# Kernel optimization log

Measured on AMD Instinct MI355X. Metric: run time of the kernel, lower is better.

The kernel has to match this reference:

```python
import jax, jax.numpy as jnp
import numpy as np

N_RAYS = 4096
WORLD_LEN = 160
K0_DIM = 12
WIDTH = 128
VIEWPE = 4
BG_LEN = 0.2
XYZ_MIN = -1.0 - BG_LEN
XYZ_MAX = 1.0 + BG_LEN
ALPHA_INIT = 1e-4
ACT_SHIFT = float(np.log(1.0 / (1.0 - ALPHA_INIT) - 1.0))  # density bias shift
BG = 1.0  # background color (render_kwargs['bg'])
DIM0 = 3 + 3 * VIEWPE * 2 + K0_DIM  # 39


def grid_interp(grid, pts):
    """Trilinear interpolation (align_corners=True). grid: [C,R,R,R], pts: [M,3] world coords -> [M,C]."""
    R = grid.shape[1]
    g = (pts - XYZ_MIN) / (XYZ_MAX - XYZ_MIN) * (R - 1)
    g = jnp.clip(g, 0.0, R - 1)
    g0 = jnp.clip(jnp.floor(g).astype(jnp.int32), 0, R - 2)
    f = g - g0
    x0, y0, z0 = g0[:, 0], g0[:, 1], g0[:, 2]
    fx, fy, fz = f[:, 0], f[:, 1], f[:, 2]

    def gat(i, j, k):
        return grid[:, i, j, k]  # [C, M]

    c00 = gat(x0, y0, z0) * (1 - fz) + gat(x0, y0, z0 + 1) * fz
    c01 = gat(x0, y0 + 1, z0) * (1 - fz) + gat(x0, y0 + 1, z0 + 1) * fz
    c10 = gat(x0 + 1, y0, z0) * (1 - fz) + gat(x0 + 1, y0, z0 + 1) * fz
    c11 = gat(x0 + 1, y0 + 1, z0) * (1 - fz) + gat(x0 + 1, y0 + 1, z0 + 1) * fz
    c0 = c00 * (1 - fy) + c01 * fy
    c1 = c10 * (1 - fy) + c11 * fy
    return (c0 * (1 - fx) + c1 * fx).T  # [M, C]


def setup_inputs() -> dict:
    key = jax.random.key(0)
    ks = jax.random.split(key, 11)
    return {
        "rays_o": jax.random.normal(ks[0], (N_RAYS, 3), jnp.float32) * 0.3,
        "rays_d": jax.random.normal(ks[1], (N_RAYS, 3), jnp.float32),
        "viewdirs": jax.random.normal(ks[2], (N_RAYS, 3), jnp.float32),
        "density_grid": jax.random.normal(ks[3], (1, WORLD_LEN, WORLD_LEN, WORLD_LEN), jnp.float32),
        "k0_grid": jax.random.normal(ks[4], (K0_DIM, WORLD_LEN, WORLD_LEN, WORLD_LEN), jnp.float32),
        "w0": jax.random.normal(ks[5], (DIM0, WIDTH), jnp.float32) * 0.05,
        "b0": jnp.zeros((WIDTH,), jnp.float32),
        "w1": jax.random.normal(ks[6], (WIDTH, WIDTH), jnp.float32) * 0.05,
        "b1": jnp.zeros((WIDTH,), jnp.float32),
        "w2": jax.random.normal(ks[7], (WIDTH, 3), jnp.float32) * 0.05,
        "b2": jnp.zeros((3,), jnp.float32),
        "stepsize": 1,
    }


def reference(rays_o, rays_d, viewdirs, density_grid, k0_grid, w0, b0, w1, b1, w2, b2, stepsize):
    sqrt3 = float(np.sqrt(3.0))
    # --- sample_ray: sample points along rays in the contracted domain ---
    N_inner = int(2.0 / (2.0 + 2.0 * BG_LEN) * sqrt3 * WORLD_LEN / stepsize) + 1
    N_outer = int(N_inner * max(0.01, BG_LEN / 2.0))
    b_inner = jnp.linspace(0.0, 2.0 * sqrt3, N_inner + 1)
    b_outer = 2.0 * sqrt3 / jnp.linspace(1.0, 0.001, N_outer + 1)
    t = jnp.concatenate([(b_inner[1:] + b_inner[:-1]) * 0.5,
                         (b_outer[1:] + b_outer[:-1]) * 0.5])  # [P]
    # scene_center = 0, scene_radius = 1 for xyz_min=-1, xyz_max=1
    rd = rays_d / jnp.linalg.norm(rays_d, axis=-1, keepdims=True)
    pts = rays_o[:, None, :] + rd[:, None, :] * t[None, :, None]  # [N,P,3]
    norm = jnp.max(jnp.abs(pts), axis=-1, keepdims=True)
    safe = jnp.maximum(norm, 1e-9)
    pts = jnp.where(norm <= 1.0, pts, pts / safe * (1.0 + BG_LEN - BG_LEN / safe))
    N, P = pts.shape[0], pts.shape[1]
    flat = pts.reshape(-1, 3)  # [M,3]

    # --- density -> alpha (Raw2Alpha); mask_cache is all-True, fast_color_thres=0 ---
    interval = float(stepsize) * 1.0  # voxel_size_ratio == 1
    dens = grid_interp(density_grid, flat)[:, 0].reshape(N, P)
    alpha = 1.0 - jnp.power(1.0 + jnp.exp(dens + ACT_SHIFT), -interval)

    # --- Alphas2Weights: per-ray alpha compositing ---
    T = jnp.cumprod(1.0 - alpha, axis=1)
    T_excl = jnp.concatenate([jnp.ones((N, 1), T.dtype), T[:, :-1]], axis=1)
    weights = alpha * T_excl  # [N,P]
    alphainv_last = T[:, -1]  # [N]

    # --- k0 features + view-dependent MLP ---
    k0 = grid_interp(k0_grid, flat).reshape(N, P, K0_DIM)
    vf = (2.0 ** jnp.arange(VIEWPE)).astype(rays_o.dtype)
    ve = (viewdirs[..., None] * vf).reshape(N, -1)
    vemb = jnp.concatenate([viewdirs, jnp.sin(ve), jnp.cos(ve)], axis=-1)  # [N, 3+24]
    feat = jnp.concatenate(
        [k0, jnp.broadcast_to(vemb[:, None, :], (N, P, vemb.shape[-1]))], axis=-1)  # [N,P,39]
    h = jax.nn.relu(feat @ w0 + b0)
    h = jax.nn.relu(h @ w1 + b1)
    rgb = jax.nn.sigmoid(h @ w2 + b2)  # [N,P,3]

    # --- volume rendering ---
    rgb_marched = jnp.sum(weights[..., None] * rgb, axis=1) + alphainv_last[:, None] * BG
    return rgb_marched  # [N,3]
```

## Files before the change

kernel.cpp:

```cpp
#include <hip/hip_runtime.h>

#define NRAYS 4096
#define PSAMP 254
#define NIN   231
#define GR    160
#define GR2   25600
#define GR3   4096000
#define SROW  136

typedef __attribute__((ext_vector_type(8))) short bf16x8;
typedef __attribute__((ext_vector_type(8))) _Float16 f16x8;
typedef __attribute__((ext_vector_type(2))) _Float16 h2;
typedef __attribute__((ext_vector_type(4))) float f32x4;

__device__ __forceinline__ unsigned short f2bf(float x) {
    union { float f; unsigned u; } v; v.f = x;
    return (unsigned short)((v.u + 0x7fffu + ((v.u >> 16) & 1u)) >> 16);
}
__device__ __forceinline__ float sigmoidf_(float x) { return 1.0f / (1.0f + __expf(-x)); }

__device__ __forceinline__ unsigned packh2(float a, float b) {
    union { _Float16 h; unsigned short u; } ua, ub;
    ua.h = (_Float16)a; ub.h = (_Float16)b;
    return (unsigned)ua.u | ((unsigned)ub.u << 16);
}
__device__ __forceinline__ float h2f(unsigned u16) {
    union { unsigned short u; _Float16 h; } v; v.u = (unsigned short)u16;
    return (float)v.h;
}
__device__ __forceinline__ unsigned pkrtz(float a, float b) {
    unsigned r;
    asm("v_cvt_pkrtz_f16_f32 %0, %1, %2" : "=v"(r) : "v"(a), "v"(b));
    return r;
}
__device__ __forceinline__ h2 u2h(unsigned u) {
    union { unsigned u; h2 h; } v; v.u = u; return v.h;
}

__global__ void prepack(const float* __restrict__ w, unsigned short* __restrict__ out,
                        int K, int N, int ldw, int NT, int KS, int f16mode) {
    const int idx = blockIdx.x * 256 + threadIdx.x;
    if (idx >= NT * KS * 64) return;
    const int l  = idx & 63, f = idx >> 6;
    const int ks = f % KS,  nt = f / KS;
    const int n  = nt * 16 + (l & 15);
    const int k0 = ks * 32 + (l >> 4) * 8;
    unsigned p[4];
    #pragma unroll
    for (int q = 0; q < 4; q++) {
        const int ka = k0 + 2 * q, kb = ka + 1;
        const float va = (ka < K && n < N) ? w[ka * ldw + n] : 0.0f;
        const float vb = (kb < K && n < N) ? w[kb * ldw + n] : 0.0f;
        p[q] = f16mode ? packh2(va, vb)
                       : ((unsigned)f2bf(va) | ((unsigned)f2bf(vb) << 16));
    }
    uint4 v; v.x = p[0]; v.y = p[1]; v.z = p[2]; v.w = p[3];
    ((uint4*)out)[idx] = v;
}

__global__ __launch_bounds__(256) void repack_grid(
    const float* __restrict__ dg, const float* __restrict__ k0g,
    unsigned short* __restrict__ pg)
{
    const int i2 = blockIdx.x * 256 + threadIdx.x;
    if (i2 >= GR3 / 2) return;
    unsigned ow[16];
    #pragma unroll
    for (int c = 0; c < 12; c += 2) {
        const float2 va = ((const float2*)(k0g + (size_t)c       * GR3))[i2];
        const float2 vb = ((const float2*)(k0g + (size_t)(c + 1) * GR3))[i2];
        ow[(c >> 1)]     = packh2(va.x, vb.x);
        ow[8 + (c >> 1)] = packh2(va.y, vb.y);
    }
    const float2 dv = ((const float2*)dg)[i2];
    ow[6]  = packh2(dv.x, 0.0f);
    ow[14] = packh2(dv.y, 0.0f);
    ow[7] = 0u; ow[15] = 0u;
    uint4* dst = (uint4*)(pg + (size_t)i2 * 32);
    dst[0] = make_uint4(ow[0],  ow[1],  ow[2],  ow[3]);
    dst[1] = make_uint4(ow[4],  ow[5],  ow[6],  ow[7]);
    dst[2] = make_uint4(ow[8],  ow[9],  ow[10], ow[11]);
    dst[3] = make_uint4(ow[12], ow[13], ow[14], ow[15]);
}

__global__ __launch_bounds__(256, 2) void voxgo_mfma_pk(
    const float* __restrict__ rays_o, const float* __restrict__ rays_d,
    const float* __restrict__ viewdirs,
    const unsigned short* __restrict__ pg,
    const float* __restrict__ b0, const float* __restrict__ b1,
    const float* __restrict__ b2,
    const unsigned short* __restrict__ pw0, const unsigned short* __restrict__ pw1,
    const unsigned short* __restrict__ pw2,
    float* __restrict__ out)
{
    const int r    = blockIdx.x;
    const int tid  = threadIdx.x;
    const int wv   = tid >> 6, lane = tid & 63, quad = lane >> 4, l16 = lane & 15;

    __shared__ unsigned short hbuf[4][64 * 128];
    __shared__ float wgt[256];
    __shared__ float redbuf[4 * 16 * 3];
    __shared__ float wtot[4];

    const float ox = rays_o[3*r+0], oy = rays_o[3*r+1], oz = rays_o[3*r+2];
    float dxv = rays_d[3*r+0], dyv = rays_d[3*r+1], dzv = rays_d[3*r+2];
    const float vdx = viewdirs[3*r+0], vdy = viewdirs[3*r+1], vdz = viewdirs[3*r+2];
    const float rinv = rsqrtf(dxv*dxv + dyv*dyv + dzv*dzv);
    dxv *= rinv; dyv *= rinv; dzv *= rinv;

    float t;
    if (tid < NIN) {
        t = ((float)tid + 0.5f) * (2.0f * 1.7320508075688772f / 231.0f);
    } else {
        const float lstep = 0.999f / 23.0f;
        const int j = tid - NIN;
        const float L0 = 1.0f - (float)j * lstep;
        const float L1 = 1.0f - (float)(j+1) * lstep;
        t = 1.7320508075688772f * (1.0f/L0 + 1.0f/L1);
    }

    float px = fmaf(dxv, t, ox), py = fmaf(dyv, t, oy), pz = fmaf(dzv, t, oz);
    const float nrm = fmaxf(fabsf(px), fmaxf(fabsf(py), fabsf(pz)));
    if (nrm > 1.0f) {
        const float s = (1.2f - 0.2f / nrm) / nrm;
        px *= s; py *= s; pz *= s;
    }

    const float gsc = 159.0f / 2.4f;
    const float gx = fminf(fmaxf((px + 1.2f) * gsc, 0.0f), 159.0f);
    const float gy = fminf(fmaxf((py + 1.2f) * gsc, 0.0f), 159.0f);
    const float gz = fminf(fmaxf((pz + 1.2f) * gsc, 0.0f), 159.0f);
    const int x0 = min((int)gx, GR-2), y0 = min((int)gy, GR-2), z0 = min((int)gz, GR-2);
    const float fx = gx - (float)x0, fy = gy - (float)y0, fz = gz - (float)z0;
    const int base = x0*GR2 + y0*GR + z0;

    const unsigned short* cp = pg + (size_t)base * 16;
    uint4 hi[8], lo[8];
    #pragma unroll
    for (int j = 0; j < 8; j++) {
        const int off = ((j >> 2) * GR2 + ((j >> 1) & 1) * GR + (j & 1)) * 16;
        hi[j] = *((const uint4*)(cp + off) + 1);
    }
    #pragma unroll
    for (int j = 0; j < 8; j++) {
        const int off = ((j >> 2) * GR2 + ((j >> 1) & 1) * GR + (j & 1)) * 16;
        lo[j] = *((const uint4*)(cp + off));
    }

    float vv[28];
    vv[0] = vdx; vv[1] = vdy; vv[2] = vdz;
    #pragma unroll
    for (int p = 0; p < 4; p++) {
        const float f = (float)(1 << p);
        vv[3+p]  = __sinf(vdx*f);  vv[7+p]  = __sinf(vdy*f);  vv[11+p] = __sinf(vdz*f);
        vv[15+p] = __cosf(vdx*f);  vv[19+p] = __cosf(vdy*f);  vv[23+p] = __cosf(vdz*f);
    }
    vv[27] = 0.0f;

    float dcr[8];
    #pragma unroll
    for (int j = 0; j < 8; j++) dcr[j] = h2f(hi[j].z & 0xffffu);
    const float c00 = dcr[0]*(1.0f-fz) + dcr[1]*fz;
    const float c01 = dcr[2]*(1.0f-fz) + dcr[3]*fz;
    const float c10 = dcr[4]*(1.0f-fz) + dcr[5]*fz;
    const float c11 = dcr[6]*(1.0f-fz) + dcr[7]*fz;
    const float dens = (c00*(1.0f-fy) + c01*fy)*(1.0f-fx) + (c10*(1.0f-fy) + c11*fy)*fx;

    const float ACT_SHIFT = -9.21024036697535f;
    const float alpha = (tid < PSAMP) ? sigmoidf_(dens + ACT_SHIFT) : 0.0f;

    float vscan = 1.0f - alpha;
    #pragma unroll
    for (int off = 1; off < 64; off <<= 1) {
        const float u = __shfl_up(vscan, off);
        if (lane >= off) vscan *= u;
    }
    if (lane == 63) wtot[wv] = vscan;
    __syncthreads();
    float pre = 1.0f;
    #pragma unroll
    for (int w = 0; w < 3; w++) if (w < wv) pre *= wtot[w];
    const float eprev = __shfl_up(vscan, 1);
    const float T_excl = (lane == 0) ? pre : pre * eprev;
    wgt[tid] = alpha * T_excl;

    const float wx0 = 1.0f-fx, wy0 = 1.0f-fy, wz0 = 1.0f-fz;
    h2 wpk[8];
    #pragma unroll
    for (int j = 0; j < 8; j++) {
        const float wj = ((j & 4) ? fx : wx0) * ((j & 2) ? fy : wy0) * ((j & 1) ? fz : wz0);
        const _Float16 wh = (_Float16)wj;
        h2 w2v; w2v[0] = wh; w2v[1] = wh; wpk[j] = w2v;
    }
    h2 ap[6];
    #pragma unroll
    for (int p = 0; p < 6; p++) { h2 z; z[0] = (_Float16)0.0f; z[1] = (_Float16)0.0f; ap[p] = z; }
    #pragma unroll
    for (int j = 0; j < 8; j++) {
        ap[0] += wpk[j] * u2h(lo[j].x);
        ap[1] += wpk[j] * u2h(lo[j].y);
        ap[2] += wpk[j] * u2h(lo[j].z);
        ap[3] += wpk[j] * u2h(lo[j].w);
        ap[4] += wpk[j] * u2h(hi[j].x);
        ap[5] += wpk[j] * u2h(hi[j].y);
    }

    unsigned fw[32];
    #pragma unroll
    for (int p = 0; p < 6; p++) { union { h2 h; unsigned u; } v; v.h = ap[p]; fw[p] = v.u; }
    #pragma unroll
    for (int i = 0; i < 14; i++) fw[6+i] = pkrtz(vv[2*i], vv[2*i+1]);
    #pragma unroll
    for (int i = 20; i < 32; i++) fw[i] = 0u;

    unsigned short* hb = &hbuf[wv][0];
    const unsigned swr = (unsigned)((l16 & 7) << 4);
    {
        const int row = tid & 63;
        const unsigned sw = (unsigned)((row & 7) << 4);
        #pragma unroll
        for (int i = 0; i < 8; i++) {
            uint4 v; v.x = fw[4*i]; v.y = fw[4*i+1]; v.z = fw[4*i+2]; v.w = fw[4*i+3];
            *(uint4*)((char*)hb + row*256 + ((unsigned)(i*16) ^ sw)) = v;
        }
    }

    f32x4 acc1[8][4];
    #pragma unroll
    for (int ft = 0; ft < 8; ft++) {
        const f32x4 bv = *(const f32x4*)(b0 + ft*16 + quad*4);
        #pragma unroll
        for (int st = 0; st < 4; st++) acc1[ft][st] = bv;
    }
    #pragma unroll
    for (int ks = 0; ks < 2; ks++) {
        f16x8 bfr[4];
        #pragma unroll
        for (int st = 0; st < 4; st++)
            bfr[st] = *(const f16x8*)((char*)hb + (st*16 + l16)*256
                                      + ((unsigned)(ks*64 + quad*16) ^ swr));
        #pragma unroll
        for (int ft = 0; ft < 8; ft++) {
            const f16x8 afr = *(const f16x8*)(pw0 + ((ft*2 + ks)*64 + lane)*8);
            #pragma unroll
            for (int st = 0; st < 4; st++)
                acc1[ft][st] = __builtin_amdgcn_mfma_f32_16x16x32_f16(afr, bfr[st], acc1[ft][st], 0,0,0);
        }
    }
    #pragma unroll
    for (int ft = 0; ft < 8; ft++)
        #pragma unroll
        for (int st = 0; st < 4; st++) {
            const f32x4 a = acc1[ft][st];
            uint2 v;
            v.x = pkrtz(fmaxf(a[0], 0.0f), fmaxf(a[1], 0.0f));
            v.y = pkrtz(fmaxf(a[2], 0.0f), fmaxf(a[3], 0.0f));
            *(uint2*)((char*)hb + (st*16 + l16)*256 + ((unsigned)(ft*32 + quad*8) ^ swr)) = v;
        }

    f32x4 acc2[8][4];
    #pragma unroll
    for (int ft = 0; ft < 8; ft++) {
        const f32x4 bv = *(const f32x4*)(b1 + ft*16 + quad*4);
        #pragma unroll
        for (int st = 0; st < 4; st++) acc2[ft][st] = bv;
    }
    #pragma unroll
    for (int ks = 0; ks < 4; ks++) {
        f16x8 bfr[4];
        #pragma unroll
        for (int st = 0; st < 4; st++)
            bfr[st] = *(const f16x8*)((char*)hb + (st*16 + l16)*256
                                      + ((unsigned)(ks*64 + quad*16) ^ swr));
        #pragma unroll
        for (int ft = 0; ft < 8; ft++) {
            const f16x8 afr = *(const f16x8*)(pw1 + ((ft*4 + ks)*64 + lane)*8);
            #pragma unroll
            for (int st = 0; st < 4; st++)
                acc2[ft][st] = __builtin_amdgcn_mfma_f32_16x16x32_f16(afr, bfr[st], acc2[ft][st], 0,0,0);
        }
    }
    #pragma unroll
    for (int ft = 0; ft < 8; ft++)
        #pragma unroll
        for (int st = 0; st < 4; st++) {
            const f32x4 a = acc2[ft][st];
            uint2 v;
            v.x = pkrtz(fmaxf(a[0], 0.0f), fmaxf(a[1], 0.0f));
            v.y = pkrtz(fmaxf(a[2], 0.0f), fmaxf(a[3], 0.0f));
            *(uint2*)((char*)hb + (st*16 + l16)*256 + ((unsigned)(ft*32 + quad*8) ^ swr)) = v;
        }

    f32x4 acc3[4];
    {
        f32x4 bz3; bz3[0] = b2[0]; bz3[1] = b2[1]; bz3[2] = b2[2]; bz3[3] = 0.0f;
        #pragma unroll
        for (int st = 0; st < 4; st++) acc3[st] = bz3;
    }
    #pragma unroll
    for (int ks = 0; ks < 4; ks++) {
        const f16x8 afr = *(const f16x8*)(pw2 + (ks*64 + lane)*8);
        #pragma unroll
        for (int st = 0; st < 4; st++) {
            const f16x8 bfr = *(const f16x8*)((char*)hb + (st*16 + l16)*256
                                              + ((unsigned)(ks*64 + quad*16) ^ swr));
            acc3[st] = __builtin_amdgcn_mfma_f32_16x16x32_f16(afr, bfr, acc3[st], 0,0,0);
        }
    }

    if (quad == 0) {
        float c0 = 0.0f, c1 = 0.0f, c2 = 0.0f;
        #pragma unroll
        for (int st = 0; st < 4; st++) {
            const float w = wgt[wv*64 + st*16 + l16];
            c0 += w * sigmoidf_(acc3[st][0]);
            c1 += w * sigmoidf_(acc3[st][1]);
            c2 += w * sigmoidf_(acc3[st][2]);
        }
        float* rb = &redbuf[(wv*16 + l16)*3];
        rb[0] = c0; rb[1] = c1; rb[2] = c2;
    }
    __syncthreads();
    if (tid < 3) {
        float acc_o = wtot[0]*wtot[1]*wtot[2]*wtot[3];
        #pragma unroll 4
        for (int i = 0; i < 64; i++) acc_o += redbuf[i*3 + tid];
        out[3*r + tid] = acc_o;
    }
}

__global__ __launch_bounds__(256, 2) void voxgo_mfma_f32(
    const float* __restrict__ rays_o, const float* __restrict__ rays_d,
    const float* __restrict__ viewdirs, const float* __restrict__ dg,
    const float* __restrict__ k0g,
    const float* __restrict__ b0, const float* __restrict__ b1,
    const float* __restrict__ b2,
    const unsigned short* __restrict__ pw0, const unsigned short* __restrict__ pw1,
    const unsigned short* __restrict__ pw2,
    float* __restrict__ out)
{
    const int r    = blockIdx.x;
    const int tid  = threadIdx.x;
    const int wv   = tid >> 6, lane = tid & 63, quad = lane >> 4, l16 = lane & 15;

    __shared__ unsigned short hbuf[4][64 * SROW];
    __shared__ float sc[256];
    __shared__ float wgt[256];
    __shared__ float redbuf[256];

    const float ox = rays_o[3*r+0], oy = rays_o[3*r+1], oz = rays_o[3*r+2];
    float dxv = rays_d[3*r+0], dyv = rays_d[3*r+1], dzv = rays_d[3*r+2];
    const float vdx = viewdirs[3*r+0], vdy = viewdirs[3*r+1], vdz = viewdirs[3*r+2];
    const float rinv = rsqrtf(dxv*dxv + dyv*dyv + dzv*dzv);
    dxv *= rinv; dyv *= rinv; dzv *= rinv;

    float t;
    if (tid < NIN) {
        t = ((float)tid + 0.5f) * (2.0f * 1.7320508075688772f / 231.0f);
    } else {
        const float lstep = 0.999f / 23.0f;
        const int j = tid - NIN;
        const float L0 = 1.0f - (float)j * lstep;
        const float L1 = 1.0f - (float)(j+1) * lstep;
        t = 1.7320508075688772f * (1.0f/L0 + 1.0f/L1);
    }

    float px = fmaf(dxv, t, ox), py = fmaf(dyv, t, oy), pz = fmaf(dzv, t, oz);
    const float nrm = fmaxf(fabsf(px), fmaxf(fabsf(py), fabsf(pz)));
    if (nrm > 1.0f) {
        const float s = (1.2f - 0.2f / nrm) / nrm;
        px *= s; py *= s; pz *= s;
    }

    const float gsc = 159.0f / 2.4f;
    const float gx = fminf(fmaxf((px + 1.2f) * gsc, 0.0f), 159.0f);
    const float gy = fminf(fmaxf((py + 1.2f) * gsc, 0.0f), 159.0f);
    const float gz = fminf(fmaxf((pz + 1.2f) * gsc, 0.0f), 159.0f);
    const int x0 = min((int)gx, GR-2), y0 = min((int)gy, GR-2), z0 = min((int)gz, GR-2);
    const float fx = gx - (float)x0, fy = gy - (float)y0, fz = gz - (float)z0;
    const int base = x0*GR2 + y0*GR + z0;

    const float d000 = dg[base],        d001 = dg[base+1];
    const float d010 = dg[base+GR],     d011 = dg[base+GR+1];
    const float d100 = dg[base+GR2],    d101 = dg[base+GR2+1];
    const float d110 = dg[base+GR2+GR], d111 = dg[base+GR2+GR+1];
    const float c00 = d000*(1.0f-fz) + d001*fz;
    const float c01 = d010*(1.0f-fz) + d011*fz;
    const float c10 = d100*(1.0f-fz) + d101*fz;
    const float c11 = d110*(1.0f-fz) + d111*fz;
    const float dens = (c00*(1.0f-fy) + c01*fy)*(1.0f-fx) + (c10*(1.0f-fy) + c11*fy)*fx;

    const float ACT_SHIFT = -9.21024036697535f;
    const float alpha = (tid < PSAMP) ? sigmoidf_(dens + ACT_SHIFT) : 0.0f;

    sc[tid] = 1.0f - alpha;
    __syncthreads();
    #pragma unroll
    for (int off = 1; off < 256; off <<= 1) {
        const float v = (tid >= off) ? sc[tid - off] : 1.0f;
        __syncthreads();
        sc[tid] *= v;
        __syncthreads();
    }
    const float T_excl = (tid == 0) ? 1.0f : sc[tid-1];
    wgt[tid] = alpha * T_excl;

    const float wx0 = 1.0f-fx, wy0 = 1.0f-fy, wz0 = 1.0f-fz;
    const float w000 = wx0*wy0*wz0, w001 = wx0*wy0*fz, w010 = wx0*fy*wz0, w011 = wx0*fy*fz;
    const float w100 = fx*wy0*wz0,  w101 = fx*wy0*fz,  w110 = fx*fy*wz0,  w111 = fx*fy*fz;

    float fv[40];
    #pragma unroll
    for (int c = 0; c < 12; c++) {
        const float* g = k0g + c*GR3 + base;
        fv[c] = w000*g[0]      + w001*g[1]
              + w010*g[GR]     + w011*g[GR+1]
              + w100*g[GR2]    + w101*g[GR2+1]
              + w110*g[GR2+GR] + w111*g[GR2+GR+1];
    }
    fv[12] = vdx; fv[13] = vdy; fv[14] = vdz;
    #pragma unroll
    for (int p = 0; p < 4; p++) {
        const float f = (float)(1 << p);
        fv[15+p] = __sinf(vdx*f);  fv[19+p] = __sinf(vdy*f);  fv[23+p] = __sinf(vdz*f);
        fv[27+p] = __cosf(vdx*f);  fv[31+p] = __cosf(vdy*f);  fv[35+p] = __cosf(vdz*f);
    }
    fv[39] = 0.0f;

    unsigned short* hb = &hbuf[wv][0];
    {
        const int row = tid & 63;
        uint4* dst = (uint4*)(hb + row * SROW);
        #pragma unroll
        for (int i = 0; i < 8; i++) {
            unsigned p[4];
            #pragma unroll
            for (int q = 0; q < 4; q++) {
                const int e0 = i*8 + 2*q, e1 = e0 + 1;
                const unsigned lov = (e0 < 39) ? f2bf(fv[e0]) : 0u;
                const unsigned hiv = (e1 < 39) ? f2bf(fv[e1]) : 0u;
                p[q] = lov | (hiv << 16);
            }
            uint4 v; v.x = p[0]; v.y = p[1]; v.z = p[2]; v.w = p[3];
            dst[i] = v;
        }
    }
    __syncthreads();

    f32x4 acc1[4][8];
    #pragma unroll
    for (int nt = 0; nt < 8; nt++) {
        const float bz = b0[nt*16 + l16];
        #pragma unroll
        for (int mt = 0; mt < 4; mt++) { f32x4 z = {bz,bz,bz,bz}; acc1[mt][nt] = z; }
    }
    #pragma unroll
    for (int ks = 0; ks < 2; ks++) {
        bf16x8 a[4];
        #pragma unroll
        for (int mt = 0; mt < 4; mt++)
            a[mt] = *(const bf16x8*)(hb + (mt*16 + l16)*SROW + ks*32 + quad*8);
        #pragma unroll
        for (int nt = 0; nt < 8; nt++) {
            const bf16x8 b = *(const bf16x8*)(pw0 + ((nt*2 + ks)*64 + lane)*8);
            #pragma unroll
            for (int mt = 0; mt < 4; mt++)
                acc1[mt][nt] = __builtin_amdgcn_mfma_f32_16x16x32_bf16(a[mt], b, acc1[mt][nt], 0,0,0);
        }
    }
    #pragma unroll
    for (int mt = 0; mt < 4; mt++)
        #pragma unroll
        for (int nt = 0; nt < 8; nt++)
            #pragma unroll
            for (int e = 0; e < 4; e++)
                hb[(mt*16 + quad*4 + e)*SROW + nt*16 + l16] = f2bf(fmaxf(acc1[mt][nt][e], 0.0f));
    __syncthreads();

    f32x4 acc2[4][8];
    #pragma unroll
    for (int nt = 0; nt < 8; nt++) {
        const float bz = b1[nt*16 + l16];
        #pragma unroll
        for (int mt = 0; mt < 4; mt++) { f32x4 z = {bz,bz,bz,bz}; acc2[mt][nt] = z; }
    }
    #pragma unroll
    for (int ks = 0; ks < 4; ks++) {
        bf16x8 a[4];
        #pragma unroll
        for (int mt = 0; mt < 4; mt++)
            a[mt] = *(const bf16x8*)(hb + (mt*16 + l16)*SROW + ks*32 + quad*8);
        #pragma unroll
        for (int nt = 0; nt < 8; nt++) {
            const bf16x8 b = *(const bf16x8*)(pw1 + ((nt*4 + ks)*64 + lane)*8);
            #pragma unroll
            for (int mt = 0; mt < 4; mt++)
                acc2[mt][nt] = __builtin_amdgcn_mfma_f32_16x16x32_bf16(a[mt], b, acc2[mt][nt], 0,0,0);
        }
    }
    #pragma unroll
    for (int mt = 0; mt < 4; mt++)
        #pragma unroll
        for (int nt = 0; nt < 8; nt++)
            #pragma unroll
            for (int e = 0; e < 4; e++)
                hb[(mt*16 + quad*4 + e)*SROW + nt*16 + l16] = f2bf(fmaxf(acc2[mt][nt][e], 0.0f));
    __syncthreads();

    f32x4 acc3[4];
    {
        const float bz = (l16 < 3) ? b2[l16] : 0.0f;
        #pragma unroll
        for (int mt = 0; mt < 4; mt++) { f32x4 z = {bz,bz,bz,bz}; acc3[mt] = z; }
    }
    #pragma unroll
    for (int ks = 0; ks < 4; ks++) {
        const bf16x8 b = *(const bf16x8*)(pw2 + (ks*64 + lane)*8);
        #pragma unroll
        for (int mt = 0; mt < 4; mt++) {
            const bf16x8 a = *(const bf16x8*)(hb + (mt*16 + l16)*SROW + ks*32 + quad*8);
            acc3[mt] = __builtin_amdgcn_mfma_f32_16x16x32_bf16(a, b, acc3[mt], 0,0,0);
        }
    }

    float contrib = 0.0f;
    #pragma unroll
    for (int mt = 0; mt < 4; mt++)
        #pragma unroll
        for (int e = 0; e < 4; e++) {
            const float s = sigmoidf_(acc3[mt][e]);
            contrib += wgt[wv*64 + mt*16 + quad*4 + e] * s;
        }
    redbuf[tid] = contrib;
    __syncthreads();
    if (tid < 3) {
        float acc_o = sc[PSAMP-1];
        #pragma unroll
        for (int w = 0; w < 4; w++)
            #pragma unroll
            for (int q = 0; q < 4; q++)
                acc_o += redbuf[w*64 + q*16 + tid];
        out[3*r + tid] = acc_o;
    }
}

extern "C" void kernel_launch(void* const* d_in, const int* in_sizes, int n_in,
                              void* d_out, int out_size, void* d_ws, size_t ws_size,
                              hipStream_t stream) {
    (void)in_sizes; (void)n_in; (void)out_size;
    const size_t PG_BYTES = (size_t)GR3 * 32;
    const size_t PW_BYTES = (size_t)(16 + 32 + 4) * 64 * 8 * 2;

    if (ws_size >= PG_BYTES + PW_BYTES) {
        unsigned short* pg  = (unsigned short*)d_ws;
        unsigned short* pw0 = (unsigned short*)((char*)d_ws + PG_BYTES);
        unsigned short* pw1 = pw0 + 16*64*8;
        unsigned short* pw2 = pw1 + 32*64*8;

        repack_grid<<<GR3/512, 256, 0, stream>>>(
            (const float*)d_in[3], (const float*)d_in[4], pg);
        prepack<<<4, 256, 0, stream>>>((const float*)d_in[5], pw0,  39, 128, 128, 8, 2, 1);
        prepack<<<8, 256, 0, stream>>>((const float*)d_in[7], pw1, 128, 128, 128, 8, 4, 1);
        prepack<<<1, 256, 0, stream>>>((const float*)d_in[9], pw2, 128,   3,   3, 1, 4, 1);

        voxgo_mfma_pk<<<NRAYS, 256, 0, stream>>>(
            (const float*)d_in[0], (const float*)d_in[1], (const float*)d_in[2],
            pg,
            (const float*)d_in[6], (const float*)d_in[8], (const float*)d_in[10],
            pw0, pw1, pw2,
            (float*)d_out);
    } else {
        unsigned short* pw0 = (unsigned short*)d_ws;
        unsigned short* pw1 = pw0 + 16*64*8;
        unsigned short* pw2 = pw1 + 32*64*8;

        prepack<<<4, 256, 0, stream>>>((const float*)d_in[5], pw0,  39, 128, 128, 8, 2, 0);
        prepack<<<8, 256, 0, stream>>>((const float*)d_in[7], pw1, 128, 128, 128, 8, 4, 0);
        prepack<<<1, 256, 0, stream>>>((const float*)d_in[9], pw2, 128,   3,   3, 1, 4, 0);

        voxgo_mfma_f32<<<NRAYS, 256, 0, stream>>>(
            (const float*)d_in[0], (const float*)d_in[1], (const float*)d_in[2],
            (const float*)d_in[3], (const float*)d_in[4],
            (const float*)d_in[6], (const float*)d_in[8], (const float*)d_in[10],
            pw0, pw1, pw2,
            (float*)d_out);
    }
}
```

Measured before the change: 440.7 us.

## Process MLP in two 32-sample halves per wave to halve LDS and registers

Each wave now runs the three-layer MFMA MLP in two passes over 32 samples instead of one pass over 64. This halves the per-wave LDS activation buffer and the accumulator register arrays, and launch bounds are raised from 2 to 4 blocks per CU to use the freed resources for higher occupancy. The cost is twice as many loads of the weight fragments from global memory, less MFMA work per weight load, and some lanes idling while each half writes its inputs.

```diff
diff --git a/kernel.cpp b/kernel.cpp
--- a/kernel.cpp
+++ b/kernel.cpp
@@ -83,7 +83,7 @@
     dst[3] = make_uint4(ow[12], ow[13], ow[14], ow[15]);
 }
 
-__global__ __launch_bounds__(256, 2) void voxgo_mfma_pk(
+__global__ __launch_bounds__(256, 4) void voxgo_mfma_pk(
     const float* __restrict__ rays_o, const float* __restrict__ rays_d,
     const float* __restrict__ viewdirs,
     const unsigned short* __restrict__ pg,
@@ -97,7 +97,7 @@
     const int tid  = threadIdx.x;
     const int wv   = tid >> 6, lane = tid & 63, quad = lane >> 4, l16 = lane & 15;
 
-    __shared__ unsigned short hbuf[4][64 * 128];
+    __shared__ unsigned short hbuf[4][32 * 128];
     __shared__ float wgt[256];
     __shared__ float redbuf[4 * 16 * 3];
     __shared__ float wtot[4];
@@ -205,120 +205,127 @@
         ap[5] += wpk[j] * u2h(hi[j].y);
     }
 
-    unsigned fw[32];
+    unsigned fw[20];
     #pragma unroll
     for (int p = 0; p < 6; p++) { union { h2 h; unsigned u; } v; v.h = ap[p]; fw[p] = v.u; }
     #pragma unroll
     for (int i = 0; i < 14; i++) fw[6+i] = pkrtz(vv[2*i], vv[2*i+1]);
-    #pragma unroll
-    for (int i = 20; i < 32; i++) fw[i] = 0u;
 
     unsigned short* hb = &hbuf[wv][0];
     const unsigned swr = (unsigned)((l16 & 7) << 4);
-    {
-        const int row = tid & 63;
-        const unsigned sw = (unsigned)((row & 7) << 4);
-        #pragma unroll
-        for (int i = 0; i < 8; i++) {
-            uint4 v; v.x = fw[4*i]; v.y = fw[4*i+1]; v.z = fw[4*i+2]; v.w = fw[4*i+3];
-            *(uint4*)((char*)hb + row*256 + ((unsigned)(i*16) ^ sw)) = v;
-        }
-    }
-
-    f32x4 acc1[8][4];
-    #pragma unroll
-    for (int ft = 0; ft < 8; ft++) {
-        const f32x4 bv = *(const f32x4*)(b0 + ft*16 + quad*4);
-        #pragma unroll
-        for (int st = 0; st < 4; st++) acc1[ft][st] = bv;
-    }
-    #pragma unroll
-    for (int ks = 0; ks < 2; ks++) {
-        f16x8 bfr[4];
-        #pragma unroll
-        for (int st = 0; st < 4; st++)
-            bfr[st] = *(const f16x8*)((char*)hb + (st*16 + l16)*256
-                                      + ((unsigned)(ks*64 + quad*16) ^ swr));
+    float cr0 = 0.0f, cr1 = 0.0f, cr2 = 0.0f;
+
+    #pragma unroll
+    for (int p = 0; p < 2; p++) {
+        if ((lane >> 5) == p) {
+            const int row = lane & 31;
+            const unsigned sw = (unsigned)((row & 7) << 4);
+            char* db = (char*)hb + row * 256;
+            #pragma unroll
+            for (int i = 0; i < 5; i++) {
+                uint4 v; v.x = fw[4*i]; v.y = fw[4*i+1]; v.z = fw[4*i+2]; v.w = fw[4*i+3];
+                *(uint4*)(db + ((unsigned)(i*16) ^ sw)) = v;
+            }
+            const uint4 z = make_uint4(0u, 0u, 0u, 0u);
+            #pragma unroll
+            for (int i = 5; i < 8; i++)
+                *(uint4*)(db + ((unsigned)(i*16) ^ sw)) = z;
+        }
+
+        f32x4 acc1[8][2];
         #pragma unroll
         for (int ft = 0; ft < 8; ft++) {
-            const f16x8 afr = *(const f16x8*)(pw0 + ((ft*2 + ks)*64 + lane)*8);
-            #pragma unroll
-            for (int st = 0; st < 4; st++)
-                acc1[ft][st] = __builtin_amdgcn_mfma_f32_16x16x32_f16(afr, bfr[st], acc1[ft][st], 0,0,0);
-        }
-    }
-    #pragma unroll
-    for (int ft = 0; ft < 8; ft++)
-        #pragma unroll
-        for (int st = 0; st < 4; st++) {
-            const f32x4 a = acc1[ft][st];
-            uint2 v;
-            v.x = pkrtz(fmaxf(a[0], 0.0f), fmaxf(a[1], 0.0f));
-            v.y = pkrtz(fmaxf(a[2], 0.0f), fmaxf(a[3], 0.0f));
-            *(uint2*)((char*)hb + (st*16 + l16)*256 + ((unsigned)(ft*32 + quad*8) ^ swr)) = v;
-        }
-
-    f32x4 acc2[8][4];
-    #pragma unroll
-    for (int ft = 0; ft < 8; ft++) {
-        const f32x4 bv = *(const f32x4*)(b1 + ft*16 + quad*4);
-        #pragma unroll
-        for (int st = 0; st < 4; st++) acc2[ft][st] = bv;
-    }
-    #pragma unroll
-    for (int ks = 0; ks < 4; ks++) {
-        f16x8 bfr[4];
-        #pragma unroll
-        for (int st = 0; st < 4; st++)
-            bfr[st] = *(const f16x8*)((char*)hb + (st*16 + l16)*256
-                                      + ((unsigned)(ks*64 + quad*16) ^ swr));
+            const f32x4 bv = *(const f32x4*)(b0 + ft*16 + quad*4);
+            acc1[ft][0] = bv; acc1[ft][1] = bv;
+        }
+        #pragma unroll
+        for (int ks = 0; ks < 2; ks++) {
+            f16x8 bfr[2];
+            #pragma unroll
+            for (int st = 0; st < 2; st++)
+                bfr[st] = *(const f16x8*)((char*)hb + (st*16 + l16)*256
+                                          + ((unsigned)(ks*64 + quad*16) ^ swr));
+            #pragma unroll
+            for (int ft = 0; ft < 8; ft++) {
+                const f16x8 afr = *(const f16x8*)(pw0 + ((ft*2 + ks)*64 + lane)*8);
+                #pragma unroll
+                for (int st = 0; st < 2; st++)
+                    acc1[ft][st] = __builtin_amdgcn_mfma_f32_16x16x32_f16(afr, bfr[st], acc1[ft][st], 0,0,0);
+            }
+        }
+        #pragma unroll
+        for (int ft = 0; ft < 8; ft++)
+            #pragma unroll
+            for (int st = 0; st < 2; st++) {
+                const f32x4 a = acc1[ft][st];
+                uint2 v;
+                v.x = pkrtz(fmaxf(a[0], 0.0f), fmaxf(a[1], 0.0f));
+                v.y = pkrtz(fmaxf(a[2], 0.0f), fmaxf(a[3], 0.0f));
+                *(uint2*)((char*)hb + (st*16 + l16)*256 + ((unsigned)(ft*32 + quad*8) ^ swr)) = v;
+            }
+
+        f32x4 acc2[8][2];
         #pragma unroll
         for (int ft = 0; ft < 8; ft++) {
-            const f16x8 afr = *(const f16x8*)(pw1 + ((ft*4 + ks)*64 + lane)*8);
-            #pragma unroll
-            for (int st = 0; st < 4; st++)
-                acc2[ft][st] = __builtin_amdgcn_mfma_f32_16x16x32_f16(afr, bfr[st], acc2[ft][st], 0,0,0);
-        }
-    }
-    #pragma unroll
-    for (int ft = 0; ft < 8; ft++)
-        #pragma unroll
-        for (int st = 0; st < 4; st++) {
-            const f32x4 a = acc2[ft][st];
-            uint2 v;
-            v.x = pkrtz(fmaxf(a[0], 0.0f), fmaxf(a[1], 0.0f));
-            v.y = pkrtz(fmaxf(a[2], 0.0f), fmaxf(a[3], 0.0f));
-            *(uint2*)((char*)hb + (st*16 + l16)*256 + ((unsigned)(ft*32 + quad*8) ^ swr)) = v;
-        }
-
-    f32x4 acc3[4];
-    {
-        f32x4 bz3; bz3[0] = b2[0]; bz3[1] = b2[1]; bz3[2] = b2[2]; bz3[3] = 0.0f;
-        #pragma unroll
-        for (int st = 0; st < 4; st++) acc3[st] = bz3;
-    }
-    #pragma unroll
-    for (int ks = 0; ks < 4; ks++) {
-        const f16x8 afr = *(const f16x8*)(pw2 + (ks*64 + lane)*8);
-        #pragma unroll
-        for (int st = 0; st < 4; st++) {
-            const f16x8 bfr = *(const f16x8*)((char*)hb + (st*16 + l16)*256
-                                              + ((unsigned)(ks*64 + quad*16) ^ swr));
-            acc3[st] = __builtin_amdgcn_mfma_f32_16x16x32_f16(afr, bfr, acc3[st], 0,0,0);
+            const f32x4 bv = *(const f32x4*)(b1 + ft*16 + quad*4);
+            acc2[ft][0] = bv; acc2[ft][1] = bv;
+        }
+        #pragma unroll
+        for (int ks = 0; ks < 4; ks++) {
+            f16x8 bfr[2];
+            #pragma unroll
+            for (int st = 0; st < 2; st++)
+                bfr[st] = *(const f16x8*)((char*)hb + (st*16 + l16)*256
+                                          + ((unsigned)(ks*64 + quad*16) ^ swr));
+            #pragma unroll
+            for (int ft = 0; ft < 8; ft++) {
+                const f16x8 afr = *(const f16x8*)(pw1 + ((ft*4 + ks)*64 + lane)*8);
+                #pragma unroll
+                for (int st = 0; st < 2; st++)
+                    acc2[ft][st] = __builtin_amdgcn_mfma_f32_16x16x32_f16(afr, bfr[st], acc2[ft][st], 0,0,0);
+            }
+        }
+        #pragma unroll
+        for (int ft = 0; ft < 8; ft++)
+            #pragma unroll
+            for (int st = 0; st < 2; st++) {
+                const f32x4 a = acc2[ft][st];
+                uint2 v;
+                v.x = pkrtz(fmaxf(a[0], 0.0f), fmaxf(a[1], 0.0f));
+                v.y = pkrtz(fmaxf(a[2], 0.0f), fmaxf(a[3], 0.0f));
+                *(uint2*)((char*)hb + (st*16 + l16)*256 + ((unsigned)(ft*32 + quad*8) ^ swr)) = v;
+            }
+
+        f32x4 acc3[2];
+        {
+            f32x4 bz3; bz3[0] = b2[0]; bz3[1] = b2[1]; bz3[2] = b2[2]; bz3[3] = 0.0f;
+            acc3[0] = bz3; acc3[1] = bz3;
+        }
+        #pragma unroll
+        for (int ks = 0; ks < 4; ks++) {
+            const f16x8 afr = *(const f16x8*)(pw2 + (ks*64 + lane)*8);
+            #pragma unroll
+            for (int st = 0; st < 2; st++) {
+                const f16x8 bfr = *(const f16x8*)((char*)hb + (st*16 + l16)*256
+                                                  + ((unsigned)(ks*64 + quad*16) ^ swr));
+                acc3[st] = __builtin_amdgcn_mfma_f32_16x16x32_f16(afr, bfr, acc3[st], 0,0,0);
+            }
+        }
+
+        if (quad == 0) {
+            #pragma unroll
+            for (int st = 0; st < 2; st++) {
+                const float w = wgt[wv*64 + p*32 + st*16 + l16];
+                cr0 += w * sigmoidf_(acc3[st][0]);
+                cr1 += w * sigmoidf_(acc3[st][1]);
+                cr2 += w * sigmoidf_(acc3[st][2]);
+            }
         }
     }
 
     if (quad == 0) {
-        float c0 = 0.0f, c1 = 0.0f, c2 = 0.0f;
-        #pragma unroll
-        for (int st = 0; st < 4; st++) {
-            const float w = wgt[wv*64 + st*16 + l16];
-            c0 += w * sigmoidf_(acc3[st][0]);
-            c1 += w * sigmoidf_(acc3[st][1]);
-            c2 += w * sigmoidf_(acc3[st][2]);
-        }
         float* rb = &redbuf[(wv*16 + l16)*3];
-        rb[0] = c0; rb[1] = c1; rb[2] = c2;
+        rb[0] = cr0; rb[1] = cr1; rb[2] = cr2;
     }
     __syncthreads();
     if (tid < 3) {
```

New measurement: 575.8 us. 1.31x slower.
